# Kernel tuning notes

Measured on AMD Instinct MI355X. Metric: run time of the kernel, lower is better.

Reference implementation:

```python
import jax, jax.numpy as jnp
import numpy as np

N_IN, N_H0, N_H1, N_H2, N_H3, N_OUT = 512, 1024, 1024, 1024, 512, 128
B, T = 128, 512
STD = 0.05


def setup_inputs() -> dict:
    key = jax.random.key(0)
    ks = jax.random.split(key, 7)
    # torch nn.Linear(in, out, bias=False) stores weight as [out, in]
    return {
        "input_spikes": jax.random.uniform(ks[0], (B, T, N_IN), dtype=jnp.float32),
        "W_in_h0": STD * jax.random.normal(ks[1], (N_H0, N_IN), dtype=jnp.float32),
        "W_h0_h1": STD * jax.random.normal(ks[2], (N_H1, N_H0), dtype=jnp.float32),
        "W_h1_h2": STD * jax.random.normal(ks[3], (N_H2, N_H1), dtype=jnp.float32),
        "W_h2_h2": STD * jax.random.normal(ks[4], (N_H2, N_H2), dtype=jnp.float32),
        "W_h2_h3": STD * jax.random.normal(ks[5], (N_H3, N_H2), dtype=jnp.float32),
        "W_h3_out": STD * jax.random.normal(ks[6], (N_OUT, N_H3), dtype=jnp.float32),
    }


def _lif(current, v, alpha, v_th):
    v = alpha * v + current
    s = (v >= v_th).astype(v.dtype)
    return s, v * (1.0 - s)


def reference(input_spikes, W_in_h0, W_h0_h1, W_h1_h2, W_h2_h2, W_h2_h3, W_h3_out):
    b = input_spikes.shape[0]
    dt = input_spikes.dtype
    z = lambda n: jnp.zeros((b, n), dtype=dt)
    # carry: membrane potentials for h0..h3, out, plus recurrent h2 spikes
    init = (z(N_H0), z(N_H1), z(N_H2), z(N_H3), z(N_OUT), z(N_H2))
    xs = jnp.swapaxes(input_spikes, 0, 1)  # [T, B, N_IN]

    def step(carry, x_t):
        v0, v1, v2, v3, vo, s2_prev = carry
        s0, v0 = _lif(x_t @ W_in_h0.T, v0, 0.9, 0.5)
        s1, v1 = _lif(s0 @ W_h0_h1.T, v1, 0.95, 0.5)
        s2, v2 = _lif(s1 @ W_h1_h2.T + s2_prev @ W_h2_h2.T, v2, 0.93, 0.5)
        s3, v3 = _lif(s2 @ W_h2_h3.T, v3, 0.9, 0.5)
        so, vo = _lif(s3 @ W_h3_out.T, vo, 0.82, 0.8)
        return (v0, v1, v2, v3, vo, s2), so

    _, out = jax.lax.scan(step, init, xs)
    output_spikes = jnp.swapaxes(out, 0, 1)  # [B, T, N_OUT]
    spike_counts = output_spikes.sum(axis=1)  # [B, N_OUT]
    return output_spikes, spike_counts
```

## Files before the change

### kernel.cpp

```cpp
#include <hip/hip_runtime.h>
#include <cstddef>


#define NB 128
#define NT 512
#define NBLK 512

enum : size_t {
  OFF_V0   = 0,
  OFF_V1   = OFF_V0 + 131072,
  OFF_V2   = OFF_V1 + 131072,
  OFF_V3   = OFF_V2 + 131072,
  OFF_VO   = OFF_V3 + 65536,
  OFF_CNT  = OFF_VO + 16384,
  OFF_C2A  = OFF_CNT + 16384,
  OFF_BYTE = OFF_C2A + 262144,
  WS_FLOATS = OFF_BYTE + 229376,
  OFF_ARR  = WS_FLOATS,
  OFF_FLAGF = OFF_ARR + 8192,
  WS_TOTAL = OFF_FLAGF + 16
};
#define BS0 0
#define BS1 262144
#define BS2 524288
#define BS3 786432

__device__ __forceinline__ void st_u16_agent(unsigned char* p, unsigned short v) {
  __hip_atomic_store((unsigned short*)p, v, __ATOMIC_RELAXED, __HIP_MEMORY_SCOPE_AGENT);
}
__device__ __forceinline__ unsigned long long ld_u64_agent(const unsigned char* p) {
  return __hip_atomic_load((const unsigned long long*)p, __ATOMIC_RELAXED, __HIP_MEMORY_SCOPE_AGENT);
}
__device__ __forceinline__ void st_u64_agent(void* p, unsigned long long v) {
  __hip_atomic_store((unsigned long long*)p, v, __ATOMIC_RELAXED, __HIP_MEMORY_SCOPE_AGENT);
}
__device__ __forceinline__ unsigned long long ld_u64_agentf(const float* p) {
  return __hip_atomic_load((const unsigned long long*)p, __ATOMIC_RELAXED, __HIP_MEMORY_SCOPE_AGENT);
}
__device__ __forceinline__ unsigned ld_u32_agent(const unsigned* p) {
  return __hip_atomic_load(p, __ATOMIC_RELAXED, __HIP_MEMORY_SCOPE_AGENT);
}
__device__ __forceinline__ void st_u32_agent(unsigned* p, unsigned v) {
  __hip_atomic_store(p, v, __ATOMIC_RELAXED, __HIP_MEMORY_SCOPE_AGENT);
}

union F2U { float2 f; unsigned long long u; };

__device__ __forceinline__ void unpack8(unsigned long long v, float* f) {
  unsigned lo = (unsigned)v, hi = (unsigned)(v >> 32);
  f[0] = (float)(lo & 0xff); f[1] = (float)((lo >> 8) & 0xff);
  f[2] = (float)((lo >> 16) & 0xff); f[3] = (float)(lo >> 24);
  f[4] = (float)(hi & 0xff); f[5] = (float)((hi >> 8) & 0xff);
  f[6] = (float)((hi >> 16) & 0xff); f[7] = (float)(hi >> 24);
}

__device__ __forceinline__ void gemm_split32(
    const unsigned char* __restrict__ Abase,
    const float* __restrict__ W,
    int bBase, int oBase, int grp, int lt,
    float* AsG, float* WsG, float acc[4][2])
{
  const int ar = lt >> 2, ac = (lt & 3) << 3;
  const int wr = lt >> 2, wk = (lt & 3) << 3;
  const int tb4 = (lt >> 4) << 2;
  const int to2 = (lt & 15) << 1;
  const int kb = grp << 9;

  const unsigned char* Arow = Abase + (size_t)(bBase + ar) * 1024 + kb + ac;
  const float* Wr = W + (size_t)(oBase + wr) * 1024 + kb + wk;

  {
    float a[8]; unpack8(ld_u64_agent(Arow), a);
    float4 w0 = *(const float4*)(Wr);
    float4 w1 = *(const float4*)(Wr + 4);
#pragma unroll
    for (int i = 0; i < 8; ++i) AsG[(ac + i) * 32 + ar] = a[i];
    WsG[(wk+0)*36+wr] = w0.x; WsG[(wk+1)*36+wr] = w0.y;
    WsG[(wk+2)*36+wr] = w0.z; WsG[(wk+3)*36+wr] = w0.w;
    WsG[(wk+4)*36+wr] = w1.x; WsG[(wk+5)*36+wr] = w1.y;
    WsG[(wk+6)*36+wr] = w1.z; WsG[(wk+7)*36+wr] = w1.w;
  }
  unsigned long long pa = ld_u64_agent(Arow + 32);
  float4 pw0 = *(const float4*)(Wr + 32);
  float4 pw1 = *(const float4*)(Wr + 36);
  __syncthreads();

  int cb = 0;
#pragma unroll 1
  for (int kt = 0; kt < 16; ++kt) {
    unsigned long long na; float4 nw0, nw1;
    if (kt + 2 < 16) {
      const int ko = (kt + 2) << 5;
      na  = ld_u64_agent(Arow + ko);
      nw0 = *(const float4*)(Wr + ko);
      nw1 = *(const float4*)(Wr + ko + 4);
    }
    const float* Asb = AsG + cb * 1024;
    const float* Wsb = WsG + cb * 1152;
#pragma unroll
    for (int k = 0; k < 32; ++k) {
      const float4 a = *(const float4*)&Asb[k * 32 + tb4];
      const float2 w = *(const float2*)&Wsb[k * 36 + to2];
      acc[0][0] = fmaf(a.x, w.x, acc[0][0]);
      acc[0][1] = fmaf(a.x, w.y, acc[0][1]);
      acc[1][0] = fmaf(a.y, w.x, acc[1][0]);
      acc[1][1] = fmaf(a.y, w.y, acc[1][1]);
      acc[2][0] = fmaf(a.z, w.x, acc[2][0]);
      acc[2][1] = fmaf(a.z, w.y, acc[2][1]);
      acc[3][0] = fmaf(a.w, w.x, acc[3][0]);
      acc[3][1] = fmaf(a.w, w.y, acc[3][1]);
    }
    if (kt + 1 < 16) {
      float* Asn = AsG + (cb ^ 1) * 1024;
      float* Wsn = WsG + (cb ^ 1) * 1152;
      float a[8]; unpack8(pa, a);
#pragma unroll
      for (int i = 0; i < 8; ++i) Asn[(ac + i) * 32 + ar] = a[i];
      Wsn[(wk+0)*36+wr] = pw0.x; Wsn[(wk+1)*36+wr] = pw0.y;
      Wsn[(wk+2)*36+wr] = pw0.z; Wsn[(wk+3)*36+wr] = pw0.w;
      Wsn[(wk+4)*36+wr] = pw1.x; Wsn[(wk+5)*36+wr] = pw1.y;
      Wsn[(wk+6)*36+wr] = pw1.z; Wsn[(wk+7)*36+wr] = pw1.w;
    }
    if (kt + 2 < 16) { pa = na; pw0 = nw0; pw1 = nw1; }
    __syncthreads();
    cb ^= 1;
  }
}

__device__ __forceinline__ void gemm_x64(
    const float* __restrict__ xrow,
    const float* __restrict__ W,
    int bBase, int oBase, int tid,
    float* As, float* Ws, float acc[4][2])
{
  const int ar = tid >> 3, ac4 = (tid & 7) << 2;
  const int wr = tid >> 2, wk = (tid & 3) << 3;
  const int tb4 = (tid >> 5) << 2;
  const int to2 = (tid & 31) << 1;
  const float* Af = xrow + (size_t)(bBase + ar) * (NT * 512) + ac4;
  const float* Wr = W + (size_t)(oBase + wr) * 512 + wk;

  {
    float4 a = *(const float4*)Af;
    float4 w0 = *(const float4*)Wr;
    float4 w1 = *(const float4*)(Wr + 4);
    As[(ac4+0)*32+ar] = a.x; As[(ac4+1)*32+ar] = a.y;
    As[(ac4+2)*32+ar] = a.z; As[(ac4+3)*32+ar] = a.w;
    Ws[(wk+0)*68+wr] = w0.x; Ws[(wk+1)*68+wr] = w0.y;
    Ws[(wk+2)*68+wr] = w0.z; Ws[(wk+3)*68+wr] = w0.w;
    Ws[(wk+4)*68+wr] = w1.x; Ws[(wk+5)*68+wr] = w1.y;
    Ws[(wk+6)*68+wr] = w1.z; Ws[(wk+7)*68+wr] = w1.w;
  }
  float4 paf = *(const float4*)(Af + 32);
  float4 pw0 = *(const float4*)(Wr + 32);
  float4 pw1 = *(const float4*)(Wr + 36);
  __syncthreads();

  int cb = 0;
#pragma unroll 1
  for (int kt = 0; kt < 16; ++kt) {
    float4 naf, nw0, nw1;
    if (kt + 2 < 16) {
      const int ko = (kt + 2) << 5;
      naf = *(const float4*)(Af + ko);
      nw0 = *(const float4*)(Wr + ko);
      nw1 = *(const float4*)(Wr + ko + 4);
    }
    const float* Asb = As + cb * 1024;
    const float* Wsb = Ws + cb * 2176;
#pragma unroll
    for (int k = 0; k < 32; ++k) {
      const float4 a = *(const float4*)&Asb[k * 32 + tb4];
      const float2 w = *(const float2*)&Wsb[k * 68 + to2];
      acc[0][0] = fmaf(a.x, w.x, acc[0][0]);
      acc[0][1] = fmaf(a.x, w.y, acc[0][1]);
      acc[1][0] = fmaf(a.y, w.x, acc[1][0]);
      acc[1][1] = fmaf(a.y, w.y, acc[1][1]);
      acc[2][0] = fmaf(a.z, w.x, acc[2][0]);
      acc[2][1] = fmaf(a.z, w.y, acc[2][1]);
      acc[3][0] = fmaf(a.w, w.x, acc[3][0]);
      acc[3][1] = fmaf(a.w, w.y, acc[3][1]);
    }
    if (kt + 1 < 16) {
      float* Asn = As + (cb ^ 1) * 1024;
      float* Wsn = Ws + (cb ^ 1) * 2176;
      Asn[(ac4+0)*32+ar] = paf.x; Asn[(ac4+1)*32+ar] = paf.y;
      Asn[(ac4+2)*32+ar] = paf.z; Asn[(ac4+3)*32+ar] = paf.w;
      Wsn[(wk+0)*68+wr] = pw0.x; Wsn[(wk+1)*68+wr] = pw0.y;
      Wsn[(wk+2)*68+wr] = pw0.z; Wsn[(wk+3)*68+wr] = pw0.w;
      Wsn[(wk+4)*68+wr] = pw1.x; Wsn[(wk+5)*68+wr] = pw1.y;
      Wsn[(wk+6)*68+wr] = pw1.z; Wsn[(wk+7)*68+wr] = pw1.w;
    }
    if (kt + 2 < 16) { paf = naf; pw0 = nw0; pw1 = nw1; }
    __syncthreads();
    cb ^= 1;
  }
}

template<bool PERSIST>
__device__ __forceinline__ void do_phase512(
    int g, int lb, int p,
    const float* __restrict__ x,
    const float* __restrict__ W0, const float* __restrict__ W1,
    const float* __restrict__ W2a, const float* __restrict__ W2b,
    const float* __restrict__ W3, const float* __restrict__ W4,
    float* __restrict__ wf, float* __restrict__ out,
    float* AsB, float* WsB, float* vpriv)
{
  unsigned char* sb = (unsigned char*)(wf + OFF_BYTE);
  float* c2a = wf + OFF_C2A;
  const int cur = p & 1, prev = cur ^ 1;
  const int tid = threadIdx.x;

  if (g == 0) {
    const int t0 = p;
    if (t0 < NT) {
      const int bBase = (lb >> 4) << 5;
      const int oBase = (lb & 15) << 6;
      float acc[4][2] = {{0.f,0.f},{0.f,0.f},{0.f,0.f},{0.f,0.f}};
      gemm_x64(x + (size_t)t0 * 512, W0, bBase, oBase, tid, AsB, WsB, acc);
      const int tb4 = (tid >> 5) << 2, to2 = (tid & 31) << 1;
      unsigned char* sOut = sb + BS0 + (size_t)cur * 131072;
      float* vg = wf + OFF_V0;
#pragma unroll
      for (int i = 0; i < 4; ++i) {
        const int b = bBase + tb4 + i;
        int si[2];
#pragma unroll
        for (int j = 0; j < 2; ++j) {
          const int o = oBase + to2 + j;
          float vold = PERSIST ? vpriv[i*2+j] : vg[(size_t)b*1024 + o];
          float vv = __fadd_rn(__fmul_rn(0.90f, vold), acc[i][j]);
          int s = (vv >= 0.5f) ? 1 : 0;
          float sf = (float)s;
          float nv = __fmul_rn(vv, __fsub_rn(1.0f, sf));
          if (PERSIST) vpriv[i*2+j] = nv; else vg[(size_t)b*1024 + o] = nv;
          si[j] = s;
        }
        st_u16_agent(sOut + (size_t)b * 1024 + oBase + to2,
                     (unsigned short)(si[0] | (si[1] << 8)));
      }
    }
    const int t4 = p - 5;
    if (t4 >= 0 && t4 < NT) {
      const int b4 = ((lb >> 4) << 5) + (tid >> 3);
      const int o4 = ((lb & 15) << 3) + (tid & 7);
      const unsigned char* a3 = sb + BS3 + (size_t)prev * 65536 + (size_t)b4 * 512;
      const float* w4r = W4 + (size_t)o4 * 512;
      float acc = 0.f;
#pragma unroll 4
      for (int kk = 0; kk < 512; kk += 8) {
        float a[8]; unpack8(ld_u64_agent(a3 + kk), a);
        float4 wA = *(const float4*)(w4r + kk);
        float4 wB = *(const float4*)(w4r + kk + 4);
        acc = fmaf(a[0], wA.x, acc);
        acc = fmaf(a[1], wA.y, acc);
        acc = fmaf(a[2], wA.z, acc);
        acc = fmaf(a[3], wA.w, acc);
        acc = fmaf(a[4], wB.x, acc);
        acc = fmaf(a[5], wB.y, acc);
        acc = fmaf(a[6], wB.z, acc);
        acc = fmaf(a[7], wB.w, acc);
      }
      float vold = PERSIST ? vpriv[8] : wf[OFF_VO + b4 * 128 + o4];
      float vv = __fadd_rn(__fmul_rn(0.82f, vold), acc);
      int s = (vv >= 0.8f) ? 1 : 0;
      float sf = (float)s;
      float nv = __fmul_rn(vv, __fsub_rn(1.0f, sf));
      if (PERSIST) vpriv[8] = nv; else wf[OFF_VO + b4 * 128 + o4] = nv;
      out[(size_t)b4 * (NT * 128) + (size_t)t4 * 128 + o4] = sf;
      if (PERSIST) vpriv[9] = __fadd_rn(vpriv[9], sf);
      else wf[OFF_CNT + b4 * 128 + o4] = __fadd_rn(wf[OFF_CNT + b4 * 128 + o4], sf);
    }
    return;
  }

  const int dt = (g == 1) ? 1 : (g == 2) ? 2 : (g == 3) ? 3 : 4;
  const int t = p - dt;
  if (t < 0 || t >= NT) return;

  const unsigned char* Ab; const float* Wm;
  switch (g) {
    case 1:  Ab = sb + BS0 + (size_t)prev * 131072; Wm = W1;  break;
    case 2:  Ab = sb + BS1 + (size_t)prev * 131072; Wm = W2a; break;
    case 3:  Ab = sb + BS2 + (size_t)prev * 131072; Wm = W2b; break;
    default: Ab = sb + BS2 + (size_t)prev * 131072; Wm = W3;  break;
  }
  const int ntO = (g == 4) ? 16 : 32;
  const int N   = (g == 4) ? 512 : 1024;
  const int bBase = (lb / ntO) << 5;
  const int oBase = (lb % ntO) << 5;
  const int grp = tid >> 7, lt = tid & 127;

  float acc[4][2] = {{0.f,0.f},{0.f,0.f},{0.f,0.f},{0.f,0.f}};
  gemm_split32(Ab, Wm, bBase, oBase, grp, lt,
               AsB + grp * 2048, WsB + grp * 2304, acc);

  float* foldp = AsB + 2048;
  if (grp == 1) {
    float4 h0, h1;
    h0.x = acc[0][0]; h0.y = acc[0][1]; h0.z = acc[1][0]; h0.w = acc[1][1];
    h1.x = acc[2][0]; h1.y = acc[2][1]; h1.z = acc[3][0]; h1.w = acc[3][1];
    *(float4*)(foldp + lt * 8) = h0;
    *(float4*)(foldp + lt * 8 + 4) = h1;
  }
  __syncthreads();
  if (grp == 0) {
    float4 h0 = *(const float4*)(foldp + lt * 8);
    float4 h1 = *(const float4*)(foldp + lt * 8 + 4);
    acc[0][0] = __fadd_rn(acc[0][0], h0.x); acc[0][1] = __fadd_rn(acc[0][1], h0.y);
    acc[1][0] = __fadd_rn(acc[1][0], h0.z); acc[1][1] = __fadd_rn(acc[1][1], h0.w);
    acc[2][0] = __fadd_rn(acc[2][0], h1.x); acc[2][1] = __fadd_rn(acc[2][1], h1.y);
    acc[3][0] = __fadd_rn(acc[3][0], h1.z); acc[3][1] = __fadd_rn(acc[3][1], h1.w);

    const int tb4 = (lt >> 4) << 2, to2 = (lt & 15) << 1;
    if (g == 2) {
      float* dst = c2a + (size_t)cur * 131072;
#pragma unroll
      for (int i = 0; i < 4; ++i) {
        const int b = bBase + tb4 + i;
        F2U u; u.f.x = acc[i][0]; u.f.y = acc[i][1];
        st_u64_agent(dst + (size_t)b * 1024 + oBase + to2, u.u);
      }
    } else {
      float alpha; float* vg; unsigned char* sOut;
      if (g == 1)      { alpha = 0.95f; vg = wf + OFF_V1; sOut = sb + BS1 + (size_t)cur * 131072; }
      else if (g == 3) { alpha = 0.93f; vg = wf + OFF_V2; sOut = sb + BS2 + (size_t)cur * 131072; }
      else             { alpha = 0.90f; vg = wf + OFF_V3; sOut = sb + BS3 + (size_t)cur * 65536;  }
      const float* c2aPrev = c2a + (size_t)prev * 131072;
#pragma unroll
      for (int i = 0; i < 4; ++i) {
        const int b = bBase + tb4 + i;
        float cin[2];
        if (g == 3) {
          F2U u; u.u = ld_u64_agentf(c2aPrev + (size_t)b * 1024 + oBase + to2);
          cin[0] = __fadd_rn(u.f.x, acc[i][0]);
          cin[1] = __fadd_rn(u.f.y, acc[i][1]);
        } else {
          cin[0] = acc[i][0]; cin[1] = acc[i][1];
        }
        int si[2];
#pragma unroll
        for (int j = 0; j < 2; ++j) {
          const int o = oBase + to2 + j;
          float vold = PERSIST ? vpriv[i*2+j] : vg[(size_t)b * N + o];
          float vv = __fadd_rn(__fmul_rn(alpha, vold), cin[j]);
          int s = (vv >= 0.5f) ? 1 : 0;
          float sf = (float)s;
          float nv = __fmul_rn(vv, __fsub_rn(1.0f, sf));
          if (PERSIST) vpriv[i*2+j] = nv; else vg[(size_t)b * N + o] = nv;
          si[j] = s;
        }
        st_u16_agent(sOut + (size_t)b * N + oBase + to2,
                     (unsigned short)(si[0] | (si[1] << 8)));
      }
    }
  }
}

__device__ __forceinline__ void phase_barrier(int p, unsigned* arr, unsigned* flag) {
  const int tid = threadIdx.x;
  __syncthreads();
  const unsigned tgt = (unsigned)(p + 1);
  if (blockIdx.x == 0) {
    if (tid == 0) st_u32_agent(arr, tgt);
    int ok;
    do {
      unsigned a0 = ld_u32_agent(arr + (tid * 2) * 16);
      unsigned a1 = ld_u32_agent(arr + (tid * 2 + 1) * 16);
      ok = __syncthreads_and((int)(a0 >= tgt && a1 >= tgt));
      if (!ok) __builtin_amdgcn_s_sleep(1);
    } while (!ok);
    if (tid == 0) st_u32_agent(flag, tgt);
    __syncthreads();
  } else {
    if (tid == 0) {
      st_u32_agent(arr + blockIdx.x * 16, tgt);
      while (ld_u32_agent(flag) < tgt) __builtin_amdgcn_s_sleep(2);
    }
    __syncthreads();
  }
}

__global__ __launch_bounds__(256) void pre_kernel(float* __restrict__ wf) {
  size_t i = (size_t)blockIdx.x * blockDim.x + threadIdx.x;
  size_t stride = (size_t)gridDim.x * blockDim.x;
  for (size_t j = i; j < WS_TOTAL; j += stride) wf[j] = 0.0f;
}

__global__ __launch_bounds__(256, 2) void persist3(
    const float* __restrict__ x,
    const float* __restrict__ W0, const float* __restrict__ W1,
    const float* __restrict__ W2a, const float* __restrict__ W2b,
    const float* __restrict__ W3, const float* __restrict__ W4,
    float* __restrict__ wf, float* __restrict__ out)
{
  __shared__ float AsB[4096];
  __shared__ float WsB[4608];
  __shared__ float vLds[256][11];
  const int tid = threadIdx.x;
  float* vpriv = &vLds[tid][0];
#pragma unroll
  for (int i = 0; i < 11; ++i) vpriv[i] = 0.0f;

  unsigned* arr  = (unsigned*)(wf + OFF_ARR);
  unsigned* flag = (unsigned*)(wf + OFF_FLAGF);

  const int blk = blockIdx.x;
  int g, lb;
  if (blk < 64)       { g = 0; lb = blk; }
  else if (blk < 192) { g = 1; lb = blk - 64; }
  else if (blk < 320) { g = 2; lb = blk - 192; }
  else if (blk < 448) { g = 3; lb = blk - 320; }
  else                { g = 4; lb = blk - 448; }

  for (int p = 0; p < NT + 5; ++p) {
    do_phase512<true>(g, lb, p, x, W0, W1, W2a, W2b, W3, W4, wf, out,
                      AsB, WsB, vpriv);
    phase_barrier(p, arr, flag);
  }

  if (g == 0) {
    const int b4 = ((lb >> 4) << 5) + (tid >> 3);
    const int o4 = ((lb & 15) << 3) + (tid & 7);
    out[(size_t)128 * NT * 128 + (size_t)b4 * 128 + o4] = vpriv[9];
  }
}


__global__ __launch_bounds__(256) void init_kernel(float* __restrict__ wf) {
  size_t i = (size_t)blockIdx.x * blockDim.x + threadIdx.x;
  size_t stride = (size_t)gridDim.x * blockDim.x;
  for (size_t j = i; j < WS_TOTAL; j += stride) wf[j] = 0.0f;
}

__global__ __launch_bounds__(256) void phase_kernel512(
    const float* __restrict__ x,
    const float* __restrict__ W0, const float* __restrict__ W1,
    const float* __restrict__ W2a, const float* __restrict__ W2b,
    const float* __restrict__ W3, const float* __restrict__ W4,
    float* __restrict__ wf, float* __restrict__ out, int p)
{
  __shared__ float AsB[4096];
  __shared__ float WsB[4608];
  const int blk = blockIdx.x;
  int g, lb;
  if (blk < 64)       { g = 0; lb = blk; }
  else if (blk < 192) { g = 1; lb = blk - 64; }
  else if (blk < 320) { g = 2; lb = blk - 192; }
  else if (blk < 448) { g = 3; lb = blk - 320; }
  else                { g = 4; lb = blk - 448; }
  float vd[11];
  do_phase512<false>(g, lb, p, x, W0, W1, W2a, W2b, W3, W4, wf, out,
                     AsB, WsB, vd);
}

__global__ __launch_bounds__(256) void fin_kernel(const float* __restrict__ counts,
                                                  float* __restrict__ out) {
  int i = blockIdx.x * blockDim.x + threadIdx.x;
  if (i < 128 * 128) out[(size_t)128 * NT * 128 + i] = counts[i];
}


extern "C" void kernel_launch(void* const* d_in, const int* in_sizes, int n_in,
                              void* d_out, int out_size, void* d_ws, size_t ws_size,
                              hipStream_t stream) {
  const float* x   = (const float*)d_in[0];
  const float* W0  = (const float*)d_in[1];
  const float* W1  = (const float*)d_in[2];
  const float* W2a = (const float*)d_in[3];
  const float* W2b = (const float*)d_in[4];
  const float* W3  = (const float*)d_in[5];
  const float* W4  = (const float*)d_in[6];
  float* wf  = (float*)d_ws;
  float* out = (float*)d_out;

  int maxBlocksPerCU = 0;
  hipError_t qe = hipOccupancyMaxActiveBlocksPerMultiprocessor(
      &maxBlocksPerCU, persist3, 256, 0);
  const bool wsOK = ws_size >= WS_TOTAL * sizeof(float);

  if (qe == hipSuccess && maxBlocksPerCU >= 2 && wsOK) {
    pre_kernel<<<256, 256, 0, stream>>>(wf);
    persist3<<<NBLK, 256, 0, stream>>>(x, W0, W1, W2a, W2b, W3, W4, wf, out);
  } else {
    (void)hipGetLastError();
    init_kernel<<<512, 256, 0, stream>>>(wf);
    for (int p = 0; p < NT + 5; ++p) {
      phase_kernel512<<<NBLK, 256, 0, stream>>>(x, W0, W1, W2a, W2b, W3, W4,
                                                wf, out, p);
    }
    fin_kernel<<<64, 256, 0, stream>>>(wf + OFF_CNT, out);
  }
}
```

Measured before the change: 19.65 ms.

## Replace global phase barrier with per-group dataflow counters and stage layer-4 spikes in LDS

```diff
diff --git a/kernel.cpp b/kernel.cpp
--- a/kernel.cpp
+++ b/kernel.cpp
@@ -17,8 +17,7 @@
   OFF_BYTE = OFF_C2A + 262144,
   WS_FLOATS = OFF_BYTE + 229376,
   OFF_ARR  = WS_FLOATS,
-  OFF_FLAGF = OFF_ARR + 8192,
-  WS_TOTAL = OFF_FLAGF + 16
+  WS_TOTAL = OFF_ARR + 512
 };
 #define BS0 0
 #define BS1 262144
@@ -39,9 +38,6 @@
 }
 __device__ __forceinline__ unsigned ld_u32_agent(const unsigned* p) {
   return __hip_atomic_load(p, __ATOMIC_RELAXED, __HIP_MEMORY_SCOPE_AGENT);
-}
-__device__ __forceinline__ void st_u32_agent(unsigned* p, unsigned v) {
-  __hip_atomic_store(p, v, __ATOMIC_RELAXED, __HIP_MEMORY_SCOPE_AGENT);
 }
 
 union F2U { float2 f; unsigned long long u; };
@@ -243,14 +239,24 @@
     }
     const int t4 = p - 5;
     if (t4 >= 0 && t4 < NT) {
-      const int b4 = ((lb >> 4) << 5) + (tid >> 3);
+      const int bBase = (lb >> 4) << 5;
+      const int b4 = bBase + (tid >> 3);
       const int o4 = ((lb & 15) << 3) + (tid & 7);
-      const unsigned char* a3 = sb + BS3 + (size_t)prev * 65536 + (size_t)b4 * 512;
+      unsigned long long* s3l = (unsigned long long*)WsB;
+      const unsigned char* s3g = sb + BS3 + (size_t)prev * 65536 + (size_t)bBase * 512;
+#pragma unroll
+      for (int i = 0; i < 8; ++i) {
+        const int idx = tid + (i << 8);
+        const int r = idx >> 6, c = idx & 63;
+        s3l[r * 65 + c] = ld_u64_agent(s3g + (size_t)idx * 8);
+      }
+      __syncthreads();
+      const unsigned long long* row = s3l + (size_t)(tid >> 3) * 65;
       const float* w4r = W4 + (size_t)o4 * 512;
       float acc = 0.f;
-#pragma unroll 4
+#pragma unroll 8
       for (int kk = 0; kk < 512; kk += 8) {
-        float a[8]; unpack8(ld_u64_agent(a3 + kk), a);
+        float a[8]; unpack8(row[kk >> 3], a);
         float4 wA = *(const float4*)(w4r + kk);
         float4 wB = *(const float4*)(w4r + kk + 4);
         acc = fmaf(a[0], wA.x, acc);
@@ -271,6 +277,7 @@
       out[(size_t)b4 * (NT * 128) + (size_t)t4 * 128 + o4] = sf;
       if (PERSIST) vpriv[9] = __fadd_rn(vpriv[9], sf);
       else wf[OFF_CNT + b4 * 128 + o4] = __fadd_rn(wf[OFF_CNT + b4 * 128 + o4], sf);
+      __syncthreads();
     }
     return;
   }
@@ -358,28 +365,8 @@
   }
 }
 
-__device__ __forceinline__ void phase_barrier(int p, unsigned* arr, unsigned* flag) {
-  const int tid = threadIdx.x;
-  __syncthreads();
-  const unsigned tgt = (unsigned)(p + 1);
-  if (blockIdx.x == 0) {
-    if (tid == 0) st_u32_agent(arr, tgt);
-    int ok;
-    do {
-      unsigned a0 = ld_u32_agent(arr + (tid * 2) * 16);
-      unsigned a1 = ld_u32_agent(arr + (tid * 2 + 1) * 16);
-      ok = __syncthreads_and((int)(a0 >= tgt && a1 >= tgt));
-      if (!ok) __builtin_amdgcn_s_sleep(1);
-    } while (!ok);
-    if (tid == 0) st_u32_agent(flag, tgt);
-    __syncthreads();
-  } else {
-    if (tid == 0) {
-      st_u32_agent(arr + blockIdx.x * 16, tgt);
-      while (ld_u32_agent(flag) < tgt) __builtin_amdgcn_s_sleep(2);
-    }
-    __syncthreads();
-  }
+__device__ __forceinline__ void df_wait(const unsigned* C, unsigned tgt) {
+  while (ld_u32_agent(C) < tgt) __builtin_amdgcn_s_sleep(2);
 }
 
 __global__ __launch_bounds__(256) void pre_kernel(float* __restrict__ wf) {
@@ -388,7 +375,7 @@
   for (size_t j = i; j < WS_TOTAL; j += stride) wf[j] = 0.0f;
 }
 
-__global__ __launch_bounds__(256, 2) void persist3(
+__global__ __launch_bounds__(256, 2) void persist4(
     const float* __restrict__ x,
     const float* __restrict__ W0, const float* __restrict__ W1,
     const float* __restrict__ W2a, const float* __restrict__ W2b,
@@ -403,8 +390,7 @@
 #pragma unroll
   for (int i = 0; i < 11; ++i) vpriv[i] = 0.0f;
 
-  unsigned* arr  = (unsigned*)(wf + OFF_ARR);
-  unsigned* flag = (unsigned*)(wf + OFF_FLAGF);
+  unsigned* C = (unsigned*)(wf + OFF_ARR);
 
   const int blk = blockIdx.x;
   int g, lb;
@@ -415,9 +401,24 @@
   else                { g = 4; lb = blk - 448; }
 
   for (int p = 0; p < NT + 5; ++p) {
+    if (tid == 0) {
+      const unsigned p128 = (unsigned)p * 128u, p64 = (unsigned)p * 64u;
+      switch (g) {
+        case 0: df_wait(C + 16, p128); df_wait(C + 64, p64);  break;
+        case 1: df_wait(C + 0,  p64);  df_wait(C + 32, p128); break;
+        case 2: df_wait(C + 16, p128); df_wait(C + 48, p128); break;
+        case 3: df_wait(C + 32, p128); df_wait(C + 48, p128);
+                df_wait(C + 64, p64);  break;
+        default: df_wait(C + 48, p128); df_wait(C + 0, p64);  break;
+      }
+    }
+    __syncthreads();
     do_phase512<true>(g, lb, p, x, W0, W1, W2a, W2b, W3, W4, wf, out,
                       AsB, WsB, vpriv);
-    phase_barrier(p, arr, flag);
+    __syncthreads();
+    if (tid == 0)
+      __hip_atomic_fetch_add(C + 16 * g, 1u, __ATOMIC_RELAXED,
+                             __HIP_MEMORY_SCOPE_AGENT);
   }
 
   if (g == 0) {
@@ -477,12 +478,12 @@
 
   int maxBlocksPerCU = 0;
   hipError_t qe = hipOccupancyMaxActiveBlocksPerMultiprocessor(
-      &maxBlocksPerCU, persist3, 256, 0);
+      &maxBlocksPerCU, persist4, 256, 0);
   const bool wsOK = ws_size >= WS_TOTAL * sizeof(float);
 
   if (qe == hipSuccess && maxBlocksPerCU >= 2 && wsOK) {
     pre_kernel<<<256, 256, 0, stream>>>(wf);
-    persist3<<<NBLK, 256, 0, stream>>>(x, W0, W1, W2a, W2b, W3, W4, wf, out);
+    persist4<<<NBLK, 256, 0, stream>>>(x, W0, W1, W2a, W2b, W3, W4, wf, out);
   } else {
     (void)hipGetLastError();
     init_kernel<<<512, 256, 0, stream>>>(wf);
```

After: 19.60 ms. No clear change (-0.2%).
